# Kernel optimization log

Measured on AMD Instinct MI355X. Metric: run time of the kernel, lower is better.

Reference implementation:

```python
import jax, jax.numpy as jnp
import numpy as np

B, NV, NH, D = 16, 1024, 1024, 1024
NEG = -1e30


def setup_inputs() -> dict:
    key = jax.random.key(0)
    ks = jax.random.split(key, 12)
    sc = 1.0 / np.sqrt(D)
    return {
        "v": jax.random.normal(ks[0], (B, NV, D), jnp.float32),
        "h": jax.random.normal(ks[1], (B, NH, D), jnp.float32),
        "z": jax.random.normal(ks[2], (B, NV, 2 * D), jnp.float32),
        "v_mask": jnp.ones((B, NV), jnp.int32),
        "h_mask": jnp.ones((B, NH), jnp.int32),
        # learned parameters (torch Linear convention: W [out,in])
        "Wv_w": jax.random.normal(ks[3], (D, D), jnp.float32) * sc,
        "Wv_b": jax.random.normal(ks[4], (D,), jnp.float32) * sc,
        "Wh_w": jax.random.normal(ks[5], (D, D), jnp.float32) * sc,
        "qv_w": jax.random.normal(ks[6], (D, D), jnp.float32) * sc,
        "qv_b": jax.random.normal(ks[7], (D,), jnp.float32) * sc,
        "kh_w": jax.random.normal(ks[8], (D, D), jnp.float32) * sc,
        "Wz_w": jax.random.normal(ks[9], (D, 2 * D), jnp.float32) * sc,
        "Wu_w": jax.random.normal(ks[10], (1, D), jnp.float32) * sc,
    }


def reference(v, h, z, v_mask, h_mask, Wv_w, Wv_b, Wh_w, qv_w, qv_b, kh_w, Wz_w, Wu_w):
    v_v = v @ Wv_w.T + Wv_b                    # [B,NV,D]
    h_h = h @ Wh_w.T                           # [B,NH,D]
    z_z = z @ Wz_w.T                           # [B,NV,D]
    query = v @ qv_w.T + qv_b                  # [B,NV,D]
    key = h @ kh_w.T                           # [B,NH,D]
    key = jnp.where(h_mask[:, :, None] == 0, NEG, key)
    att = jnp.einsum('bqd,bkd->bqk', query, key)       # [B,NV,NH]
    h_v = jnp.einsum('bqk,bkd->bqd', jax.nn.softmax(att, axis=-1), h_h)
    s = jax.nn.sigmoid(v_v + h_v + z_z)        # [B,NV,D]
    # W_u(s_i + s_j) == u_i + u_j since W_u is linear with no bias
    u = jnp.einsum('bnd,d->bn', s, Wu_w[0])    # [B,NV]
    f = u[:, :, None] + u[:, None, :]          # [B,NV,NV] pairwise scores
    f = jnp.where(v_mask[:, None, :] == 0, NEG, f)
    f = jnp.einsum('bij,bjd->bid', jax.nn.softmax(f, axis=-1), v)  # [B,NV,D]
    h_new = f
    z_new = jnp.concatenate((s, f), axis=-1)   # [B,NV,2D]
    return h_new, z_new
```

## Files before the change

kernel.cpp:

```cpp
#include <hip/hip_runtime.h>

#define BB 16
#define NV 1024
#define NH 1024
#define DD 1024

typedef _Float16 f16x8 __attribute__((ext_vector_type(8)));
typedef _Float16 f16x4 __attribute__((ext_vector_type(4)));
typedef float f32x4 __attribute__((ext_vector_type(4)));

__global__ __launch_bounds__(256) void cast_k(const float* __restrict__ in,
                                              _Float16* __restrict__ out, long n4) {
  long i = (long)blockIdx.x * 256 + threadIdx.x;
  long stride = (long)gridDim.x * 256;
  for (; i < n4; i += stride) {
    float4 x = ((const float4*)in)[i];
    f16x4 o;
    o[0] = (_Float16)x.x; o[1] = (_Float16)x.y;
    o[2] = (_Float16)x.z; o[3] = (_Float16)x.w;
    ((f16x4*)out)[i] = o;
  }
}

__global__ __launch_bounds__(256) void split_k(const float* __restrict__ in,
                                               _Float16* __restrict__ hi,
                                               _Float16* __restrict__ lo, long n4) {
  long i = (long)blockIdx.x * 256 + threadIdx.x;
  long stride = (long)gridDim.x * 256;
  for (; i < n4; i += stride) {
    float4 x = ((const float4*)in)[i];
    f16x4 h, l;
    h[0] = (_Float16)x.x; h[1] = (_Float16)x.y;
    h[2] = (_Float16)x.z; h[3] = (_Float16)x.w;
    l[0] = (_Float16)(x.x - (float)h[0]);
    l[1] = (_Float16)(x.y - (float)h[1]);
    l[2] = (_Float16)(x.z - (float)h[2]);
    l[3] = (_Float16)(x.w - (float)h[3]);
    ((f16x4*)hi)[i] = h;
    ((f16x4*)lo)[i] = l;
  }
}

__device__ inline void gl_lds16(const _Float16* g, _Float16* l) {
  __builtin_amdgcn_global_load_lds((__attribute__((address_space(1))) void*)g,
                                   (__attribute__((address_space(3))) void*)l,
                                   16, 0, 0);
}

__device__ inline void decode256(int flat, int NB, int& bm, int& bn, int& bz) {
  int xcd = flat & 7, j = flat >> 3;
  if (NB == 1) {
    bz = 0;
    bm = xcd * 8 + (j >> 2);
    bn = j & 3;
  } else {
    bz = xcd * 2 + (j >> 4);
    int r = j & 15;
    bm = r >> 2;
    bn = r & 3;
  }
}


template <typename CT>
__global__ __launch_bounds__(512) void gemm256_nt_k(
    const _Float16* __restrict__ A, const _Float16* __restrict__ B,
    CT* __restrict__ C, const float* __restrict__ bias,
    int K, int NB, long sA, long sB, long sC) {
  __shared__ _Float16 lds[65536];
  const int tid = threadIdx.x;
  const int w = tid >> 6, l = tid & 63;
  int bm, bn, bz;
  decode256(blockIdx.x, NB, bm, bn, bz);
  const _Float16* Ab = A + (long)bz * sA;
  const _Float16* Bb = B + (long)bz * sB;
  CT* Cb = C + (long)bz * sC;

  const int srow = w * 16 + (l >> 2);
  const int sslot = (l & 3) ^ ((l >> 3) & 3);
  const _Float16* gA = Ab + (long)(bm * 256 + srow) * K + sslot * 8;
  const _Float16* gB = Bb + (long)(bn * 256 + srow) * K + sslot * 8;
  const long rs128 = (long)128 * K;
  const int T = K >> 5;

  const int fr = l & 15, fq = l >> 4;
  const int sw = (fr >> 1) & 3;
  const int wm = w >> 2, wn = w & 3;
  const int aoff = (wm * 128 + fr) * 32 + (fq ^ sw) * 8;
  const int boff = (wn * 64 + fr) * 32 + (fq ^ sw) * 8;

  f32x4 acc[8][4] = {};

  auto stage = [&](int st) {
    _Float16* dA = lds + (st & 3) * 16384 + w * 512;
    _Float16* dB = dA + 8192;
    const _Float16* pA = gA + st * 32;
    const _Float16* pB = gB + st * 32;
    gl_lds16(pA, dA);
    gl_lds16(pA + rs128, dA + 4096);
    gl_lds16(pB, dB);
    gl_lds16(pB + rs128, dB + 4096);
  };

  stage(0); stage(1); stage(2);
  asm volatile("s_waitcnt vmcnt(8)" ::: "memory");
  __builtin_amdgcn_s_barrier();
  __builtin_amdgcn_sched_barrier(0);

  for (int t = 0; t < T; ++t) {
    const _Float16* bufA = lds + (t & 3) * 16384;
    const _Float16* bufB = bufA + 8192;
    if (t + 3 < T) stage(t + 3);
    f16x8 bf[4], af[4];
#pragma unroll
    for (int n = 0; n < 4; ++n) bf[n] = *(const f16x8*)&bufB[boff + n * 512];
#pragma unroll
    for (int m = 0; m < 4; ++m) af[m] = *(const f16x8*)&bufA[aoff + m * 512];
    __builtin_amdgcn_s_setprio(1);
#pragma unroll
    for (int m = 0; m < 4; ++m)
#pragma unroll
      for (int n = 0; n < 4; ++n)
        acc[m][n] = __builtin_amdgcn_mfma_f32_16x16x32_f16(af[m], bf[n], acc[m][n], 0, 0, 0);
    __builtin_amdgcn_s_setprio(0);
#pragma unroll
    for (int m = 0; m < 4; ++m) af[m] = *(const f16x8*)&bufA[aoff + (m + 4) * 512];
    __builtin_amdgcn_s_setprio(1);
#pragma unroll
    for (int m = 0; m < 4; ++m)
#pragma unroll
      for (int n = 0; n < 4; ++n)
        acc[m + 4][n] = __builtin_amdgcn_mfma_f32_16x16x32_f16(af[m], bf[n], acc[m + 4][n], 0, 0, 0);
    __builtin_amdgcn_s_setprio(0);
    if (t + 1 < T) {
      const int hi = (t + 3 < T) ? t + 3 : T - 1;
      const int cnt = 4 * (hi - (t + 1));
      if (cnt >= 8)      asm volatile("s_waitcnt vmcnt(8)" ::: "memory");
      else if (cnt == 4) asm volatile("s_waitcnt vmcnt(4)" ::: "memory");
      else               asm volatile("s_waitcnt vmcnt(0)" ::: "memory");
      __builtin_amdgcn_s_barrier();
      __builtin_amdgcn_sched_barrier(0);
    }
  }

#pragma unroll
  for (int m = 0; m < 8; ++m) {
    const int grow = bm * 256 + wm * 128 + m * 16 + fq * 4;
#pragma unroll
    for (int n = 0; n < 4; ++n) {
      const int gcol = bn * 256 + wn * 64 + n * 16 + fr;
      const float bv = bias ? bias[gcol] : 0.0f;
#pragma unroll
      for (int e = 0; e < 4; ++e)
        Cb[(long)(grow + e) * 1024 + gcol] = (CT)(acc[m][n][e] + bv);
    }
  }
}

template <bool SPLIT_OUT>
__global__ __launch_bounds__(512) void gemm3_256_k(
    const _Float16* __restrict__ Ahi, const _Float16* __restrict__ Alo,
    const _Float16* __restrict__ Bhi, const _Float16* __restrict__ Blo,
    float* __restrict__ Cf, _Float16* __restrict__ Chi, _Float16* __restrict__ Clo,
    const float* __restrict__ bias, const int* __restrict__ mask,
    int K, int NB, long sA, long sB, long sC) {
  __shared__ _Float16 lds[65536];
  const int tid = threadIdx.x;
  const int w = tid >> 6, l = tid & 63;
  int bm, bn, bz;
  decode256(blockIdx.x, NB, bm, bn, bz);

  const int srow = w * 16 + (l >> 2);
  const int sslot = (l & 3) ^ ((l >> 3) & 3);
  const long abase = (long)(bm * 256 + srow) * K + sslot * 8 + (long)bz * sA;
  const long bbase = (long)(bn * 256 + srow) * K + sslot * 8 + (long)bz * sB;
  const _Float16* gAh = Ahi + abase;
  const _Float16* gAl = Alo + abase;
  const _Float16* gBh = Bhi + bbase;
  const _Float16* gBl = Blo + bbase;
  const long rs128 = (long)128 * K;
  const int T = K >> 5;

  const int fr = l & 15, fq = l >> 4;
  const int sw = (fr >> 1) & 3;
  const int wm = w >> 2, wn = w & 3;
  const int aoff = (wm * 128 + fr) * 32 + (fq ^ sw) * 8;
  const int boff = (wn * 64 + fr) * 32 + (fq ^ sw) * 8;

  f32x4 acc[8][4] = {};

  auto stage = [&](int st) {
    _Float16* d = lds + (st & 1) * 32768 + w * 512;
    const int ko = st * 32;
    gl_lds16(gAh + ko, d);
    gl_lds16(gAh + ko + rs128, d + 4096);
    gl_lds16(gAl + ko, d + 8192);
    gl_lds16(gAl + ko + rs128, d + 12288);
    gl_lds16(gBh + ko, d + 16384);
    gl_lds16(gBh + ko + rs128, d + 20480);
    gl_lds16(gBl + ko, d + 24576);
    gl_lds16(gBl + ko + rs128, d + 28672);
  };

  stage(0); stage(1);
  asm volatile("s_waitcnt vmcnt(8)" ::: "memory");
  __builtin_amdgcn_s_barrier();
  __builtin_amdgcn_sched_barrier(0);

  for (int t = 0; t < T; ++t) {
    const _Float16* bA = lds + (t & 1) * 32768;
    const _Float16* bB = bA + 16384;
    f16x8 bh[4], bl[4], ah[4], al[4];
#pragma unroll
    for (int n = 0; n < 4; ++n) {
      bh[n] = *(const f16x8*)&bB[boff + n * 512];
      bl[n] = *(const f16x8*)&bB[8192 + boff + n * 512];
    }
#pragma unroll
    for (int m = 0; m < 4; ++m) {
      ah[m] = *(const f16x8*)&bA[aoff + m * 512];
      al[m] = *(const f16x8*)&bA[8192 + aoff + m * 512];
    }
    __builtin_amdgcn_s_setprio(1);
#pragma unroll
    for (int m = 0; m < 4; ++m)
#pragma unroll
      for (int n = 0; n < 4; ++n) {
        acc[m][n] = __builtin_amdgcn_mfma_f32_16x16x32_f16(ah[m], bh[n], acc[m][n], 0, 0, 0);
        acc[m][n] = __builtin_amdgcn_mfma_f32_16x16x32_f16(al[m], bh[n], acc[m][n], 0, 0, 0);
        acc[m][n] = __builtin_amdgcn_mfma_f32_16x16x32_f16(ah[m], bl[n], acc[m][n], 0, 0, 0);
      }
    __builtin_amdgcn_s_setprio(0);
#pragma unroll
    for (int m = 0; m < 4; ++m) {
      ah[m] = *(const f16x8*)&bA[aoff + (m + 4) * 512];
      al[m] = *(const f16x8*)&bA[8192 + aoff + (m + 4) * 512];
    }
    asm volatile("s_waitcnt lgkmcnt(0)" ::: "memory");
    __builtin_amdgcn_s_barrier();
    __builtin_amdgcn_sched_barrier(0);
    if (t + 2 < T) stage(t + 2);
    __builtin_amdgcn_s_setprio(1);
#pragma unroll
    for (int m = 0; m < 4; ++m)
#pragma unroll
      for (int n = 0; n < 4; ++n) {
        acc[m + 4][n] = __builtin_amdgcn_mfma_f32_16x16x32_f16(ah[m], bh[n], acc[m + 4][n], 0, 0, 0);
        acc[m + 4][n] = __builtin_amdgcn_mfma_f32_16x16x32_f16(al[m], bh[n], acc[m + 4][n], 0, 0, 0);
        acc[m + 4][n] = __builtin_amdgcn_mfma_f32_16x16x32_f16(ah[m], bl[n], acc[m + 4][n], 0, 0, 0);
      }
    __builtin_amdgcn_s_setprio(0);
    if (t + 1 < T) {
      if (t + 2 < T) asm volatile("s_waitcnt vmcnt(8)" ::: "memory");
      else           asm volatile("s_waitcnt vmcnt(0)" ::: "memory");
      __builtin_amdgcn_s_barrier();
      __builtin_amdgcn_sched_barrier(0);
    }
  }

#pragma unroll
  for (int m = 0; m < 8; ++m) {
    const int grow = bm * 256 + wm * 128 + m * 16 + fq * 4;
#pragma unroll
    for (int n = 0; n < 4; ++n) {
      const int gcol = bn * 256 + wn * 64 + n * 16 + fr;
      const float bv = bias ? bias[gcol] : 0.0f;
#pragma unroll
      for (int e = 0; e < 4; ++e) {
        float val = acc[m][n][e] + bv;
        if (mask && mask[grow + e] == 0) val = -30000.0f;
        const long idx = (long)(grow + e) * 1024 + gcol + (long)bz * sC;
        if (SPLIT_OUT) {
          _Float16 hi = (_Float16)val;
          Chi[idx] = hi;
          Clo[idx] = (_Float16)(val - (float)hi);
        } else {
          Cf[idx] = val;
        }
      }
    }
  }
}

__device__ inline float wave_max(float v) {
#pragma unroll
  for (int o = 32; o > 0; o >>= 1) v = fmaxf(v, __shfl_xor(v, o, 64));
  return v;
}
__device__ inline float wave_sum(float v) {
#pragma unroll
  for (int o = 32; o > 0; o >>= 1) v += __shfl_xor(v, o, 64);
  return v;
}

__global__ __launch_bounds__(256) void softmax_rows_k(const float* __restrict__ att,
                                                      _Float16* __restrict__ P) {
  __shared__ float red[4];
  long row = blockIdx.x;
  int t = threadIdx.x, w = t >> 6;
  float4 x = ((const float4*)(att + row * 1024))[t];
  float m = fmaxf(fmaxf(x.x, x.y), fmaxf(x.z, x.w));
  m = wave_max(m);
  if ((t & 63) == 0) red[w] = m;
  __syncthreads();
  m = fmaxf(fmaxf(red[0], red[1]), fmaxf(red[2], red[3]));
  float e0 = expf(x.x - m), e1 = expf(x.y - m), e2 = expf(x.z - m), e3 = expf(x.w - m);
  float s = wave_sum(e0 + e1 + e2 + e3);
  __syncthreads();
  if ((t & 63) == 0) red[w] = s;
  __syncthreads();
  float inv = 1.0f / (red[0] + red[1] + red[2] + red[3]);
  f16x4 o;
  o[0] = (_Float16)(e0 * inv); o[1] = (_Float16)(e1 * inv);
  o[2] = (_Float16)(e2 * inv); o[3] = (_Float16)(e3 * inv);
  ((f16x4*)(P + row * 1024))[t] = o;
}

__global__ __launch_bounds__(256) void s_u_k(const _Float16* __restrict__ Vv,
                                             const float* __restrict__ Hv,
                                             const _Float16* __restrict__ Zz,
                                             const float* __restrict__ Wu,
                                             float* __restrict__ zout,
                                             float* __restrict__ u) {
  __shared__ float red[4];
  long row = blockIdx.x;
  int t = threadIdx.x, w = t >> 6;
  f16x4 a = ((const f16x4*)(Vv + row * 1024))[t];
  float4 b = ((const float4*)(Hv + row * 1024))[t];
  f16x4 c = ((const f16x4*)(Zz + row * 1024))[t];
  float4 wu = ((const float4*)Wu)[t];
  float4 sv;
  sv.x = 1.0f / (1.0f + expf(-((float)a[0] + b.x + (float)c[0])));
  sv.y = 1.0f / (1.0f + expf(-((float)a[1] + b.y + (float)c[1])));
  sv.z = 1.0f / (1.0f + expf(-((float)a[2] + b.z + (float)c[2])));
  sv.w = 1.0f / (1.0f + expf(-((float)a[3] + b.w + (float)c[3])));
  ((float4*)(zout + row * 2048))[t] = sv;
  float part = sv.x * wu.x + sv.y * wu.y + sv.z * wu.z + sv.w * wu.w;
  part = wave_sum(part);
  if ((t & 63) == 0) red[w] = part;
  __syncthreads();
  if (t == 0) u[row] = red[0] + red[1] + red[2] + red[3];
}

__global__ __launch_bounds__(256) void u_softmax_k(const float* __restrict__ u,
                                                   const int* __restrict__ vmask,
                                                   float* __restrict__ p) {
  __shared__ float red[4];
  int b = blockIdx.x, t = threadIdx.x, w = t >> 6;
  float4 uv = ((const float4*)(u + b * 1024))[t];
  int4 mv = ((const int4*)(vmask + b * 1024))[t];
  float l0 = mv.x ? uv.x : -1e30f;
  float l1 = mv.y ? uv.y : -1e30f;
  float l2 = mv.z ? uv.z : -1e30f;
  float l3 = mv.w ? uv.w : -1e30f;
  float m = wave_max(fmaxf(fmaxf(l0, l1), fmaxf(l2, l3)));
  if ((t & 63) == 0) red[w] = m;
  __syncthreads();
  m = fmaxf(fmaxf(red[0], red[1]), fmaxf(red[2], red[3]));
  float e0 = expf(l0 - m), e1 = expf(l1 - m), e2 = expf(l2 - m), e3 = expf(l3 - m);
  float s = wave_sum(e0 + e1 + e2 + e3);
  __syncthreads();
  if ((t & 63) == 0) red[w] = s;
  __syncthreads();
  float inv = 1.0f / (red[0] + red[1] + red[2] + red[3]);
  float4 o = make_float4(e0 * inv, e1 * inv, e2 * inv, e3 * inv);
  ((float4*)(p + b * 1024))[t] = o;
}

__global__ __launch_bounds__(256) void f_part_k(const float* __restrict__ p,
                                               const float* __restrict__ v,
                                               float* __restrict__ f) {
  int d = blockIdx.x * 256 + threadIdx.x;
  int b = blockIdx.y;
  int jc = blockIdx.z;
  const float* vb = v + ((long)b * NV + jc * 128) * DD + d;
  const float* pb = p + b * NV + jc * 128;
  float acc = 0.0f;
#pragma unroll 4
  for (int j = 0; j < 128; ++j) acc = fmaf(pb[j], vb[(long)j * DD], acc);
  atomicAdd(&f[b * DD + d], acc);
}

__global__ __launch_bounds__(256) void bcast_k(const float* __restrict__ f,
                                               float* __restrict__ hout,
                                               float* __restrict__ zout) {
  long idx = (long)blockIdx.x * 256 + threadIdx.x;
  int d4 = (int)(idx & 255);
  long bn = idx >> 8;
  int b = (int)(bn >> 10);
  float4 val = ((const float4*)f)[(b << 8) + d4];
  ((float4*)hout)[idx] = val;
  ((float4*)zout)[bn * 512 + 256 + d4] = val;
}

extern "C" void kernel_launch(void* const* d_in, const int* in_sizes, int n_in,
                              void* d_out, int out_size, void* d_ws, size_t ws_size,
                              hipStream_t stream) {
  const float* v = (const float*)d_in[0];
  const float* h = (const float*)d_in[1];
  const float* z = (const float*)d_in[2];
  const int* v_mask = (const int*)d_in[3];
  const int* h_mask = (const int*)d_in[4];
  const float* Wv_w = (const float*)d_in[5];
  const float* Wv_b = (const float*)d_in[6];
  const float* Wh_w = (const float*)d_in[7];
  const float* qv_w = (const float*)d_in[8];
  const float* qv_b = (const float*)d_in[9];
  const float* kh_w = (const float*)d_in[10];
  const float* Wz_w = (const float*)d_in[11];
  const float* Wu_w = (const float*)d_in[12];

  float* h_new = (float*)d_out;
  float* z_new = (float*)d_out + (long)BB * NV * DD;

  const size_t MB = 1u << 20;
  char* W = (char*)d_ws;
  _Float16* vhi  = (_Float16*)(W + 0 * MB);
  _Float16* vlo  = (_Float16*)(W + 32 * MB);
  _Float16* P16  = (_Float16*)(W + 32 * MB);
  _Float16* hhi  = (_Float16*)(W + 64 * MB);
  _Float16* hlo  = (_Float16*)(W + 96 * MB);
  _Float16* Hht16 = (_Float16*)(W + 96 * MB);
  _Float16* z16  = (_Float16*)(W + 128 * MB);
  _Float16* qvhi = (_Float16*)(W + 192 * MB);
  _Float16* qvlo = (_Float16*)(W + 194 * MB);
  _Float16* khhi = (_Float16*)(W + 196 * MB);
  _Float16* khlo = (_Float16*)(W + 198 * MB);
  _Float16* Wv16 = (_Float16*)(W + 200 * MB);
  _Float16* Wh16 = (_Float16*)(W + 202 * MB);
  _Float16* Wz16 = (_Float16*)(W + 204 * MB);
  _Float16* Qhi  = (_Float16*)(W + 208 * MB);
  _Float16* Vv16 = (_Float16*)(W + 208 * MB);
  _Float16* Qlo  = (_Float16*)(W + 240 * MB);
  _Float16* Zz16 = (_Float16*)(W + 240 * MB);
  _Float16* Khi  = (_Float16*)(W + 272 * MB);
  _Float16* Klo  = (_Float16*)(W + 304 * MB);
  float*    Hv32 = (float*)(W + 272 * MB);
  float*    att32 = (float*)(W + 336 * MB);
  float*    u_buf = (float*)(W + 400 * MB);
  float*    p_buf = (float*)(W + 400 * MB + 65536);
  float*    f_buf = (float*)(W + 400 * MB + 2 * 65536);

  const long nVD = (long)BB * NV * DD;
  const long s1M = (long)NV * DD;

  auto cast = [&](const float* src, _Float16* dst, long n) {
    long n4 = n / 4;
    cast_k<<<(int)((n4 + 255) / 256), 256, 0, stream>>>(src, dst, n4);
  };
  auto split = [&](const float* src, _Float16* hi, _Float16* lo, long n) {
    long n4 = n / 4;
    split_k<<<(int)((n4 + 255) / 256), 256, 0, stream>>>(src, hi, lo, n4);
  };

  split(v, vhi, vlo, nVD);
  split(h, hhi, hlo, nVD);
  cast(z, z16, nVD * 2);
  split(qv_w, qvhi, qvlo, (long)DD * DD);
  split(kh_w, khhi, khlo, (long)DD * DD);
  cast(Wv_w, Wv16, (long)DD * DD);
  cast(Wh_w, Wh16, (long)DD * DD);
  cast(Wz_w, Wz16, (long)DD * 2 * DD);

  gemm3_256_k<true><<<256, 512, 0, stream>>>(vhi, vlo, qvhi, qvlo,
      nullptr, Qhi, Qlo, qv_b, nullptr, DD, 1, 0, 0, 0);
  gemm3_256_k<true><<<256, 512, 0, stream>>>(hhi, hlo, khhi, khlo,
      nullptr, Khi, Klo, nullptr, h_mask, DD, 1, 0, 0, 0);
  gemm3_256_k<false><<<256, 512, 0, stream>>>(Qhi, Qlo, Khi, Klo,
      att32, nullptr, nullptr, nullptr, nullptr, DD, BB, s1M, s1M, s1M);
  softmax_rows_k<<<BB * NV, 256, 0, stream>>>(att32, P16);
  gemm256_nt_k<_Float16><<<256, 512, 0, stream>>>(Wh16, hhi, Hht16, nullptr, DD, BB, 0, s1M, s1M);
  gemm256_nt_k<_Float16><<<256, 512, 0, stream>>>(vhi, Wv16, Vv16, Wv_b, DD, 1, 0, 0, 0);
  gemm256_nt_k<_Float16><<<256, 512, 0, stream>>>(z16, Wz16, Zz16, nullptr, 2 * DD, 1, 0, 0, 0);
  gemm256_nt_k<float><<<256, 512, 0, stream>>>(P16, Hht16, Hv32, nullptr, NH, BB, s1M, s1M, s1M);
  s_u_k<<<BB * NV, 256, 0, stream>>>(Vv16, Hv32, Zz16, Wu_w, z_new, u_buf);
  u_softmax_k<<<BB, 256, 0, stream>>>(u_buf, v_mask, p_buf);
  hipMemsetAsync(f_buf, 0, (long)BB * DD * 4, stream);
  f_part_k<<<dim3(4, BB, 8), 256, 0, stream>>>(p_buf, v, f_buf);
  bcast_k<<<(int)(nVD / 4 / 256), 256, 0, stream>>>(f_buf, h_new, z_new);
}
```

Baseline: 1.027 ms.

## Interleave split A/B global-to-LDS prefetch with finer MFMA groups in GEMM loops

Splits the per-stage global-to-LDS loads into separate A and B halves and spreads them across the K-iteration, placing each between smaller groups of MFMAs separated by sched barriers. In the 4-buffer GEMM, a mid-iteration block barrier is added before the next stage is issued. The goal is to keep memory traffic flowing while the matrix units are busy, instead of issuing the whole stage in one burst. The costs are an extra barrier, more live fragment registers (af[8], ah/al[8]), and tighter sensitivity to the vmcnt wait counts.

```diff
diff --git a/kernel.cpp b/kernel.cpp
--- a/kernel.cpp
+++ b/kernel.cpp
@@ -91,18 +91,20 @@
 
   f32x4 acc[8][4] = {};
 
-  auto stage = [&](int st) {
+  auto stageA = [&](int st) {
     _Float16* dA = lds + (st & 3) * 16384 + w * 512;
-    _Float16* dB = dA + 8192;
     const _Float16* pA = gA + st * 32;
-    const _Float16* pB = gB + st * 32;
     gl_lds16(pA, dA);
     gl_lds16(pA + rs128, dA + 4096);
+  };
+  auto stageB = [&](int st) {
+    _Float16* dB = lds + (st & 3) * 16384 + 8192 + w * 512;
+    const _Float16* pB = gB + st * 32;
     gl_lds16(pB, dB);
     gl_lds16(pB + rs128, dB + 4096);
   };
 
-  stage(0); stage(1); stage(2);
+  stageA(0); stageB(0); stageA(1); stageB(1); stageA(2); stageB(2);
   asm volatile("s_waitcnt vmcnt(8)" ::: "memory");
   __builtin_amdgcn_s_barrier();
   __builtin_amdgcn_sched_barrier(0);
@@ -110,27 +112,50 @@
   for (int t = 0; t < T; ++t) {
     const _Float16* bufA = lds + (t & 3) * 16384;
     const _Float16* bufB = bufA + 8192;
-    if (t + 3 < T) stage(t + 3);
-    f16x8 bf[4], af[4];
+    f16x8 af[8], bf[4];
 #pragma unroll
     for (int n = 0; n < 4; ++n) bf[n] = *(const f16x8*)&bufB[boff + n * 512];
 #pragma unroll
-    for (int m = 0; m < 4; ++m) af[m] = *(const f16x8*)&bufA[aoff + m * 512];
-    __builtin_amdgcn_s_setprio(1);
-#pragma unroll
-    for (int m = 0; m < 4; ++m)
+    for (int m = 0; m < 2; ++m) af[m] = *(const f16x8*)&bufA[aoff + m * 512];
+    __builtin_amdgcn_s_setprio(1);
+#pragma unroll
+    for (int m = 0; m < 2; ++m)
 #pragma unroll
       for (int n = 0; n < 4; ++n)
         acc[m][n] = __builtin_amdgcn_mfma_f32_16x16x32_f16(af[m], bf[n], acc[m][n], 0, 0, 0);
     __builtin_amdgcn_s_setprio(0);
-#pragma unroll
-    for (int m = 0; m < 4; ++m) af[m] = *(const f16x8*)&bufA[aoff + (m + 4) * 512];
-    __builtin_amdgcn_s_setprio(1);
-#pragma unroll
-    for (int m = 0; m < 4; ++m)
+    __builtin_amdgcn_sched_barrier(0);
+#pragma unroll
+    for (int m = 2; m < 4; ++m) af[m] = *(const f16x8*)&bufA[aoff + m * 512];
+    __builtin_amdgcn_s_setprio(1);
+#pragma unroll
+    for (int m = 2; m < 4; ++m)
 #pragma unroll
       for (int n = 0; n < 4; ++n)
-        acc[m + 4][n] = __builtin_amdgcn_mfma_f32_16x16x32_f16(af[m], bf[n], acc[m + 4][n], 0, 0, 0);
+        acc[m][n] = __builtin_amdgcn_mfma_f32_16x16x32_f16(af[m], bf[n], acc[m][n], 0, 0, 0);
+    __builtin_amdgcn_s_setprio(0);
+    __builtin_amdgcn_s_barrier();
+    __builtin_amdgcn_sched_barrier(0);
+#pragma unroll
+    for (int m = 4; m < 6; ++m) af[m] = *(const f16x8*)&bufA[aoff + m * 512];
+    if (t + 3 < T) stageA(t + 3);
+    __builtin_amdgcn_s_setprio(1);
+#pragma unroll
+    for (int m = 4; m < 6; ++m)
+#pragma unroll
+      for (int n = 0; n < 4; ++n)
+        acc[m][n] = __builtin_amdgcn_mfma_f32_16x16x32_f16(af[m], bf[n], acc[m][n], 0, 0, 0);
+    __builtin_amdgcn_s_setprio(0);
+    __builtin_amdgcn_sched_barrier(0);
+#pragma unroll
+    for (int m = 6; m < 8; ++m) af[m] = *(const f16x8*)&bufA[aoff + m * 512];
+    if (t + 3 < T) stageB(t + 3);
+    __builtin_amdgcn_s_setprio(1);
+#pragma unroll
+    for (int m = 6; m < 8; ++m)
+#pragma unroll
+      for (int n = 0; n < 4; ++n)
+        acc[m][n] = __builtin_amdgcn_mfma_f32_16x16x32_f16(af[m], bf[n], acc[m][n], 0, 0, 0);
     __builtin_amdgcn_s_setprio(0);
     if (t + 1 < T) {
       const int hi = (t + 3 < T) ? t + 3 : T - 1;
@@ -189,20 +214,24 @@
 
   f32x4 acc[8][4] = {};
 
-  auto stage = [&](int st) {
+  auto stageA3 = [&](int st) {
     _Float16* d = lds + (st & 1) * 32768 + w * 512;
     const int ko = st * 32;
     gl_lds16(gAh + ko, d);
     gl_lds16(gAh + ko + rs128, d + 4096);
     gl_lds16(gAl + ko, d + 8192);
     gl_lds16(gAl + ko + rs128, d + 12288);
+  };
+  auto stageB3 = [&](int st) {
+    _Float16* d = lds + (st & 1) * 32768 + w * 512;
+    const int ko = st * 32;
     gl_lds16(gBh + ko, d + 16384);
     gl_lds16(gBh + ko + rs128, d + 20480);
     gl_lds16(gBl + ko, d + 24576);
     gl_lds16(gBl + ko + rs128, d + 28672);
   };
 
-  stage(0); stage(1);
+  stageA3(0); stageB3(0); stageA3(1); stageB3(1);
   asm volatile("s_waitcnt vmcnt(8)" ::: "memory");
   __builtin_amdgcn_s_barrier();
   __builtin_amdgcn_sched_barrier(0);
@@ -210,7 +239,7 @@
   for (int t = 0; t < T; ++t) {
     const _Float16* bA = lds + (t & 1) * 32768;
     const _Float16* bB = bA + 16384;
-    f16x8 bh[4], bl[4], ah[4], al[4];
+    f16x8 ah[8], al[8], bh[4], bl[4];
 #pragma unroll
     for (int n = 0; n < 4; ++n) {
       bh[n] = *(const f16x8*)&bB[boff + n * 512];
@@ -223,7 +252,7 @@
     }
     __builtin_amdgcn_s_setprio(1);
 #pragma unroll
-    for (int m = 0; m < 4; ++m)
+    for (int m = 0; m < 2; ++m)
 #pragma unroll
       for (int n = 0; n < 4; ++n) {
         acc[m][n] = __builtin_amdgcn_mfma_f32_16x16x32_f16(ah[m], bh[n], acc[m][n], 0, 0, 0);
@@ -231,23 +260,46 @@
         acc[m][n] = __builtin_amdgcn_mfma_f32_16x16x32_f16(ah[m], bl[n], acc[m][n], 0, 0, 0);
       }
     __builtin_amdgcn_s_setprio(0);
-#pragma unroll
-    for (int m = 0; m < 4; ++m) {
-      ah[m] = *(const f16x8*)&bA[aoff + (m + 4) * 512];
-      al[m] = *(const f16x8*)&bA[8192 + aoff + (m + 4) * 512];
-    }
+    __builtin_amdgcn_sched_barrier(0);
+#pragma unroll
+    for (int m = 4; m < 8; ++m) {
+      ah[m] = *(const f16x8*)&bA[aoff + m * 512];
+      al[m] = *(const f16x8*)&bA[8192 + aoff + m * 512];
+    }
+    __builtin_amdgcn_s_setprio(1);
+#pragma unroll
+    for (int m = 2; m < 4; ++m)
+#pragma unroll
+      for (int n = 0; n < 4; ++n) {
+        acc[m][n] = __builtin_amdgcn_mfma_f32_16x16x32_f16(ah[m], bh[n], acc[m][n], 0, 0, 0);
+        acc[m][n] = __builtin_amdgcn_mfma_f32_16x16x32_f16(al[m], bh[n], acc[m][n], 0, 0, 0);
+        acc[m][n] = __builtin_amdgcn_mfma_f32_16x16x32_f16(ah[m], bl[n], acc[m][n], 0, 0, 0);
+      }
+    __builtin_amdgcn_s_setprio(0);
     asm volatile("s_waitcnt lgkmcnt(0)" ::: "memory");
     __builtin_amdgcn_s_barrier();
     __builtin_amdgcn_sched_barrier(0);
-    if (t + 2 < T) stage(t + 2);
-    __builtin_amdgcn_s_setprio(1);
-#pragma unroll
-    for (int m = 0; m < 4; ++m)
+    if (t + 2 < T) stageA3(t + 2);
+    __builtin_amdgcn_s_setprio(1);
+#pragma unroll
+    for (int m = 4; m < 6; ++m)
 #pragma unroll
       for (int n = 0; n < 4; ++n) {
-        acc[m + 4][n] = __builtin_amdgcn_mfma_f32_16x16x32_f16(ah[m], bh[n], acc[m + 4][n], 0, 0, 0);
-        acc[m + 4][n] = __builtin_amdgcn_mfma_f32_16x16x32_f16(al[m], bh[n], acc[m + 4][n], 0, 0, 0);
-        acc[m + 4][n] = __builtin_amdgcn_mfma_f32_16x16x32_f16(ah[m], bl[n], acc[m + 4][n], 0, 0, 0);
+        acc[m][n] = __builtin_amdgcn_mfma_f32_16x16x32_f16(ah[m], bh[n], acc[m][n], 0, 0, 0);
+        acc[m][n] = __builtin_amdgcn_mfma_f32_16x16x32_f16(al[m], bh[n], acc[m][n], 0, 0, 0);
+        acc[m][n] = __builtin_amdgcn_mfma_f32_16x16x32_f16(ah[m], bl[n], acc[m][n], 0, 0, 0);
+      }
+    __builtin_amdgcn_s_setprio(0);
+    __builtin_amdgcn_sched_barrier(0);
+    if (t + 2 < T) stageB3(t + 2);
+    __builtin_amdgcn_s_setprio(1);
+#pragma unroll
+    for (int m = 6; m < 8; ++m)
+#pragma unroll
+      for (int n = 0; n < 4; ++n) {
+        acc[m][n] = __builtin_amdgcn_mfma_f32_16x16x32_f16(ah[m], bh[n], acc[m][n], 0, 0, 0);
+        acc[m][n] = __builtin_amdgcn_mfma_f32_16x16x32_f16(al[m], bh[n], acc[m][n], 0, 0, 0);
+        acc[m][n] = __builtin_amdgcn_mfma_f32_16x16x32_f16(ah[m], bl[n], acc[m][n], 0, 0, 0);
       }
     __builtin_amdgcn_s_setprio(0);
     if (t + 1 < T) {
```

Result: no change. 1.023 ms (-0.3%).
